# Kernel optimization log

Measured on AMD Instinct MI355X. Metric: run time of the kernel, lower is better.

Reference implementation:

```python
import jax, jax.numpy as jnp
import numpy as np
from jax import lax

B, T, I, H = 256, 256, 512, 512


def setup_inputs() -> dict:
    key = jax.random.key(0)
    ks = jax.random.split(key, 7)
    s = 1.0 / np.sqrt(H)
    return {
        "x": jax.random.normal(ks[0], (B, T, I), dtype=jnp.float32),
        "W_ih": jax.random.normal(ks[1], (4 * H, I), dtype=jnp.float32) * s,
        "W_hh": jax.random.normal(ks[2], (4 * H, H), dtype=jnp.float32) * s,
        "b_ih": jax.random.normal(ks[3], (4 * H,), dtype=jnp.float32) * s,
        "b_hh": jax.random.normal(ks[4], (4 * H,), dtype=jnp.float32) * s,
        "fc_w": jax.random.normal(ks[5], (1, H), dtype=jnp.float32) * s,
        "fc_b": jax.random.normal(ks[6], (1,), dtype=jnp.float32) * s,
    }


def reference(x, W_ih, W_hh, b_ih, b_hh, fc_w, fc_b):
    # x: [B, T, I]. Single-layer LSTM (PyTorch gate order i,f,g,o), zero init state.
    Bh = x.shape[0]
    Hd = W_hh.shape[1]
    # Precompute input contribution for all timesteps: [B, T, 4H]
    xg = jnp.einsum('bti,gi->btg', x, W_ih) + b_ih + b_hh

    def step(carry, xt):
        h, c = carry
        g = xt + h @ W_hh.T  # [B, 4H]
        i = jax.nn.sigmoid(g[:, :Hd])
        f = jax.nn.sigmoid(g[:, Hd:2 * Hd])
        gg = jnp.tanh(g[:, 2 * Hd:3 * Hd])
        o = jax.nn.sigmoid(g[:, 3 * Hd:])
        c_new = f * c + i * gg
        h_new = o * jnp.tanh(c_new)
        return (h_new, c_new), None

    h0 = jnp.zeros((Bh, Hd), dtype=x.dtype)
    c0 = jnp.zeros((Bh, Hd), dtype=x.dtype)
    (h_last, _), _ = lax.scan(step, (h0, c0), jnp.swapaxes(xg, 0, 1))
    # Final linear head on last timestep: [B, 1]
    return h_last @ fc_w.T + fc_b
```

## Files before the change

kernel.cpp:

```cpp
#include <hip/hip_runtime.h>

#define BDIM 256
#define TDIM 256
#define IDIM 512
#define HDIM 512
#define G4   2048

typedef __attribute__((ext_vector_type(4))) float f32x4;
typedef __attribute__((ext_vector_type(8))) short short8;
typedef __attribute__((ext_vector_type(8))) unsigned short u16x8;
typedef __attribute__((ext_vector_type(4))) unsigned short u16x4;
typedef unsigned long long ull;

__device__ __forceinline__ unsigned short f2bf(float f) {
  union { float f; unsigned u; } v; v.f = f;
  unsigned r = v.u + 0x7FFFu + ((v.u >> 16) & 1u);
  return (unsigned short)(r >> 16);
}
__device__ __forceinline__ float bf2f(unsigned short h) {
  union { unsigned u; float f; } v; v.u = ((unsigned)h) << 16; return v.f;
}
__device__ __forceinline__ float sigmoidf_fast(float x) {
  return 1.0f / (1.0f + __expf(-x));
}
__device__ __forceinline__ float tanhf_fast(float x) {
  float e = __expf(2.0f * x);
  return 1.0f - 2.0f / (e + 1.0f);
}
__device__ __forceinline__ void gl_lds16(const unsigned short* g, unsigned short* l) {
  __builtin_amdgcn_global_load_lds(
      (const __attribute__((address_space(1))) unsigned int*)g,
      (__attribute__((address_space(3))) unsigned int*)l, 16, 0, 0);
}

__device__ __forceinline__ size_t xg_off(int m, int n) {
  int b = m >> 8, t = m & 255;
  int q = n >> 9, jcol = n & 511;
  return (((size_t)t * 8 + (b >> 5)) * 8 + (jcol >> 6)) * 8192
         + (size_t)q * 2048 + (b & 31) * 64 + (jcol & 63);
}

__global__ void __launch_bounds__(256) convert_bf16(
    const float* __restrict__ x, const float* __restrict__ w,
    unsigned short* __restrict__ xb, unsigned short* __restrict__ wb)
{
  const size_t NX8 = (size_t)BDIM * TDIM * IDIM / 8;
  const size_t NW8 = (size_t)G4 * IDIM / 8;
  size_t idx = (size_t)blockIdx.x * 256 + threadIdx.x;
  const float4* sp; u16x8* dp; size_t i;
  if (idx < NX8)      { sp = (const float4*)x; dp = (u16x8*)xb; i = idx; }
  else if (idx < NX8 + NW8) { sp = (const float4*)w; dp = (u16x8*)wb; i = idx - NX8; }
  else return;
  float4 a = sp[i * 2], b = sp[i * 2 + 1];
  u16x8 o = { f2bf(a.x), f2bf(a.y), f2bf(a.z), f2bf(a.w),
              f2bf(b.x), f2bf(b.y), f2bf(b.z), f2bf(b.w) };
  dp[i] = o;
}

__global__ void __launch_bounds__(256, 2) xg_gemm_bf16(
    const unsigned short* __restrict__ Xb, const unsigned short* __restrict__ Wb,
    const float* __restrict__ b_ih, const float* __restrict__ b_hh,
    unsigned short* __restrict__ xg)
{
  __shared__ unsigned short sA[128 * 32];
  __shared__ unsigned short sB[128 * 32];

  const int tid  = threadIdx.x;
  const int lane = tid & 63;
  const int wave = tid >> 6;
  const int l15  = lane & 15;
  const int quad = lane >> 4;
  const int nt = blockIdx.x & 15;
  const int mt = blockIdx.x >> 4;
  const int wm = (wave >> 1) * 64;
  const int wn = (wave & 1) * 64;

  f32x4 acc[4][4];
  #pragma unroll
  for (int i = 0; i < 4; ++i)
    #pragma unroll
    for (int j = 0; j < 4; ++j)
      acc[i][j] = (f32x4){0.f, 0.f, 0.f, 0.f};

  for (int kt = 0; kt < 16; ++kt) {
    #pragma unroll
    for (int i = 0; i < 2; ++i) {
      int c   = wave * 128 + i * 64 + lane;
      int row = c >> 2, cg = c & 3;
      const unsigned short* ga = Xb + (size_t)(mt * 128 + row) * 512 + kt * 32 + cg * 8;
      gl_lds16(ga, sA + (size_t)(wave * 128 + i * 64) * 8);
      const unsigned short* gb = Wb + (size_t)(nt * 128 + row) * 512 + kt * 32 + cg * 8;
      gl_lds16(gb, sB + (size_t)(wave * 128 + i * 64) * 8);
    }
    __syncthreads();

    short8 af[4], bfr[4];
    #pragma unroll
    for (int i = 0; i < 4; ++i) {
      af[i]  = *(const short8*)&sA[(wm + i * 16 + l15) * 32 + quad * 8];
      bfr[i] = *(const short8*)&sB[(wn + i * 16 + l15) * 32 + quad * 8];
    }
    #pragma unroll
    for (int am = 0; am < 4; ++am)
      #pragma unroll
      for (int an = 0; an < 4; ++an)
        acc[am][an] = __builtin_amdgcn_mfma_f32_16x16x32_bf16(
            af[am], bfr[an], acc[am][an], 0, 0, 0);
    __syncthreads();
  }

  float biasv[4];
  #pragma unroll
  for (int an = 0; an < 4; ++an) {
    int n = nt * 128 + wn + an * 16 + l15;
    biasv[an] = b_ih[n] + b_hh[n];
  }
  #pragma unroll
  for (int am = 0; am < 4; ++am)
    #pragma unroll
    for (int reg = 0; reg < 4; ++reg) {
      int m = mt * 128 + wm + am * 16 + quad * 4 + reg;
      #pragma unroll
      for (int an = 0; an < 4; ++an) {
        int n = nt * 128 + wn + an * 16 + l15;
        xg[xg_off(m, n)] = f2bf(acc[am][an][reg] + biasv[an]);
      }
    }
}

__global__ void __launch_bounds__(256, 2) xg_gemm_f32(
    const float* __restrict__ X, const float* __restrict__ Wih,
    const float* __restrict__ b_ih, const float* __restrict__ b_hh,
    unsigned short* __restrict__ xg)
{
  __shared__ unsigned short sA[128][40];
  __shared__ unsigned short sB[128][40];

  const int tid  = threadIdx.x;
  const int lane = tid & 63;
  const int wave = tid >> 6;
  const int l15  = lane & 15;
  const int quad = lane >> 4;
  const int nt = blockIdx.x;
  const int mt = blockIdx.y;
  const int wm = (wave >> 1) * 64;
  const int wn = (wave & 1) * 64;
  const int r    = tid >> 1;
  const int half = (tid & 1) * 16;

  const float* arow = X   + (size_t)(mt * 128 + r) * 512 + half;
  const float* brow = Wih + (size_t)(nt * 128 + r) * 512 + half;

  f32x4 acc[4][4];
  #pragma unroll
  for (int i = 0; i < 4; ++i)
    #pragma unroll
    for (int j = 0; j < 4; ++j)
      acc[i][j] = (f32x4){0.f, 0.f, 0.f, 0.f};

  for (int kt = 0; kt < 16; ++kt) {
    const float* ap = arow + kt * 32;
    const float* bp = brow + kt * 32;
    #pragma unroll
    for (int i = 0; i < 4; ++i) {
      float4 a = ((const float4*)ap)[i];
      u16x4 av = { f2bf(a.x), f2bf(a.y), f2bf(a.z), f2bf(a.w) };
      *(u16x4*)&sA[r][half + i * 4] = av;
      float4 b = ((const float4*)bp)[i];
      u16x4 bv = { f2bf(b.x), f2bf(b.y), f2bf(b.z), f2bf(b.w) };
      *(u16x4*)&sB[r][half + i * 4] = bv;
    }
    __syncthreads();
    short8 af[4], bfr[4];
    #pragma unroll
    for (int i = 0; i < 4; ++i) {
      af[i]  = *(const short8*)&sA[wm + i * 16 + l15][quad * 8];
      bfr[i] = *(const short8*)&sB[wn + i * 16 + l15][quad * 8];
    }
    #pragma unroll
    for (int am = 0; am < 4; ++am)
      #pragma unroll
      for (int an = 0; an < 4; ++an)
        acc[am][an] = __builtin_amdgcn_mfma_f32_16x16x32_bf16(
            af[am], bfr[an], acc[am][an], 0, 0, 0);
    __syncthreads();
  }

  float biasv[4];
  #pragma unroll
  for (int an = 0; an < 4; ++an) {
    int n = nt * 128 + wn + an * 16 + l15;
    biasv[an] = b_ih[n] + b_hh[n];
  }
  #pragma unroll
  for (int am = 0; am < 4; ++am)
    #pragma unroll
    for (int reg = 0; reg < 4; ++reg) {
      int m = mt * 128 + wm + am * 16 + quad * 4 + reg;
      #pragma unroll
      for (int an = 0; an < 4; ++an) {
        int n = nt * 128 + wn + an * 16 + l15;
        xg[xg_off(m, n)] = f2bf(acc[am][an][reg] + biasv[an]);
      }
    }
}

__global__ void __launch_bounds__(512, 2) lstm_scan(
    const float* __restrict__ Whh, const unsigned short* __restrict__ xg,
    unsigned short* __restrict__ hbuf0, unsigned short* __restrict__ hbuf1,
    unsigned int* __restrict__ flags)
{
  __shared__ unsigned short sH[32][520];
  __shared__ float sG[32][260];

  const int tid  = threadIdx.x;
  const int lane = tid & 63;
  const int wave = tid >> 6;
  const int l15  = lane & 15;
  const int quad = lane >> 4;
  const int q    = wave >> 1;
  const int np   = (wave & 1) * 2;
  const int bb = blockIdx.x >> 3;
  const int jw = blockIdx.x & 7;
  const int bbase = bb * 32;
  const int jbase = jw * 64;

  short8 bfrag[2][16];
  #pragma unroll
  for (int n2 = 0; n2 < 2; ++n2) {
    const float* wrow = Whh + (size_t)(q * 512 + jbase + (np + n2) * 16 + l15) * 512;
    #pragma unroll
    for (int ks = 0; ks < 16; ++ks) {
      const float* p = wrow + ks * 32 + quad * 8;
      float4 f0 = ((const float4*)p)[0];
      float4 f1 = ((const float4*)p)[1];
      short8 v;
      v[0] = (short)f2bf(f0.x); v[1] = (short)f2bf(f0.y);
      v[2] = (short)f2bf(f0.z); v[3] = (short)f2bf(f0.w);
      v[4] = (short)f2bf(f1.x); v[5] = (short)f2bf(f1.y);
      v[6] = (short)f2bf(f1.z); v[7] = (short)f2bf(f1.w);
      bfrag[n2][ks] = v;
    }
  }

  const int r  = tid >> 4;
  const int j0 = (tid & 15) * 4;
  float c[4] = {0.f, 0.f, 0.f, 0.f};
  unsigned int* flagbase = flags + bb * 32;

  for (int t = 0; t < TDIM; ++t) {
    const unsigned short* hsrc = (t & 1) ? hbuf1 : hbuf0;
    unsigned short* hdst = (t & 1) ? hbuf0 : hbuf1;

    const unsigned short* xgb = xg + (((size_t)t * 8 + bb) * 8 + jw) * 8192;
    ull xv64[4];
    #pragma unroll
    for (int qq = 0; qq < 4; ++qq)
      xv64[qq] = *(const ull*)(xgb + qq * 2048 + r * 64 + j0);

    if (t > 0 && wave == 0) {
      const unsigned int* fp = flagbase + (lane & 7);
      int guard = 0;
      for (;;) {
        unsigned v = __hip_atomic_load(fp, __ATOMIC_RELAXED, __HIP_MEMORY_SCOPE_AGENT);
        bool ok = (lane >= 8) || (v >= (unsigned)t);
        if ((__ballot(ok) & 0xFFull) == 0xFFull) break;
        if (++guard > (1 << 21)) break;
        __builtin_amdgcn_s_sleep(1);
      }
    }
    __syncthreads();

    const ull* src = (const ull*)hsrc + (size_t)bbase * 128;
    ull hv[8];
    #pragma unroll
    for (int i = 0; i < 8; ++i)
      hv[i] = __hip_atomic_load(src + i * 512 + tid, __ATOMIC_RELAXED,
                                __HIP_MEMORY_SCOPE_AGENT);
    #pragma unroll
    for (int i = 0; i < 8; ++i) {
      int idx = i * 512 + tid;
      *(ull*)&sH[idx >> 7][(idx & 127) * 4] = hv[i];
    }
    __syncthreads();

    f32x4 acc[2][2];
    acc[0][0] = acc[0][1] = acc[1][0] = acc[1][1] = (f32x4){0.f,0.f,0.f,0.f};
    #pragma unroll
    for (int ks = 0; ks < 16; ++ks) {
      int koff = ks * 32 + quad * 8;
      short8 a0 = *(const short8*)&sH[l15][koff];
      short8 a1 = *(const short8*)&sH[16 + l15][koff];
      acc[0][0] = __builtin_amdgcn_mfma_f32_16x16x32_bf16(a0, bfrag[0][ks], acc[0][0], 0, 0, 0);
      acc[1][0] = __builtin_amdgcn_mfma_f32_16x16x32_bf16(a1, bfrag[0][ks], acc[1][0], 0, 0, 0);
      acc[0][1] = __builtin_amdgcn_mfma_f32_16x16x32_bf16(a0, bfrag[1][ks], acc[0][1], 0, 0, 0);
      acc[1][1] = __builtin_amdgcn_mfma_f32_16x16x32_bf16(a1, bfrag[1][ks], acc[1][1], 0, 0, 0);
    }
    #pragma unroll
    for (int m = 0; m < 2; ++m)
      #pragma unroll
      for (int n2 = 0; n2 < 2; ++n2) {
        int col = q * 64 + (np + n2) * 16 + l15;
        #pragma unroll
        for (int rr = 0; rr < 4; ++rr)
          sG[m * 16 + quad * 4 + rr][col] = acc[m][n2][rr];
      }
    __syncthreads();

    {
      float4 GI = *(const float4*)&sG[r][j0];
      float4 GF = *(const float4*)&sG[r][64 + j0];
      float4 GG = *(const float4*)&sG[r][128 + j0];
      float4 GO = *(const float4*)&sG[r][192 + j0];
      u16x4 xi  = __builtin_bit_cast(u16x4, xv64[0]);
      u16x4 xf  = __builtin_bit_cast(u16x4, xv64[1]);
      u16x4 xgv = __builtin_bit_cast(u16x4, xv64[2]);
      u16x4 xo  = __builtin_bit_cast(u16x4, xv64[3]);
      float gi[4] = {GI.x, GI.y, GI.z, GI.w};
      float gf[4] = {GF.x, GF.y, GF.z, GF.w};
      float gg[4] = {GG.x, GG.y, GG.z, GG.w};
      float go[4] = {GO.x, GO.y, GO.z, GO.w};
      float h4[4];
      #pragma unroll
      for (int k = 0; k < 4; ++k) {
        float vi = sigmoidf_fast(gi[k] + bf2f(xi[k]));
        float vf = sigmoidf_fast(gf[k] + bf2f(xf[k]));
        float vg = tanhf_fast   (gg[k] + bf2f(xgv[k]));
        float vo = sigmoidf_fast(go[k] + bf2f(xo[k]));
        c[k] = vf * c[k] + vi * vg;
        h4[k] = vo * tanhf_fast(c[k]);
      }
      ull hvout = (ull)f2bf(h4[0])
                | ((ull)f2bf(h4[1]) << 16)
                | ((ull)f2bf(h4[2]) << 32)
                | ((ull)f2bf(h4[3]) << 48);
      __hip_atomic_store((ull*)hdst + (size_t)(bbase + r) * 128 + (jbase + j0) / 4,
                         hvout, __ATOMIC_RELAXED, __HIP_MEMORY_SCOPE_AGENT);
    }

    __syncthreads();
    if (tid == 0)
      __hip_atomic_store(flagbase + jw, (unsigned)(t + 1), __ATOMIC_RELAXED,
                         __HIP_MEMORY_SCOPE_AGENT);
  }
}

__global__ void head_kernel(const unsigned short* __restrict__ h,
                            const float* __restrict__ fc_w,
                            const float* __restrict__ fc_b,
                            float* __restrict__ out)
{
  const int b = blockIdx.x;
  const int lane = threadIdx.x;
  const unsigned short* hr = h + (size_t)b * 512;
  float s = 0.f;
  #pragma unroll
  for (int i = 0; i < 8; ++i) {
    int idx = lane + i * 64;
    s += bf2f(hr[idx]) * fc_w[idx];
  }
  #pragma unroll
  for (int off = 32; off > 0; off >>= 1) s += __shfl_down(s, off);
  if (lane == 0) out[b] = s + fc_b[0];
}

extern "C" void kernel_launch(void* const* d_in, const int* in_sizes, int n_in,
                              void* d_out, int out_size, void* d_ws, size_t ws_size,
                              hipStream_t stream) {
  const float* x    = (const float*)d_in[0];
  const float* W_ih = (const float*)d_in[1];
  const float* W_hh = (const float*)d_in[2];
  const float* b_ih = (const float*)d_in[3];
  const float* b_hh = (const float*)d_in[4];
  const float* fc_w = (const float*)d_in[5];
  const float* fc_b = (const float*)d_in[6];
  float* out = (float*)d_out;

  const size_t XG = (size_t)BDIM * TDIM * G4 * 2;
  const size_t HB = (size_t)BDIM * HDIM * 2;
  char* ws = (char*)d_ws;
  unsigned short* xg    = (unsigned short*)ws;
  unsigned short* hbuf0 = (unsigned short*)(ws + XG);
  unsigned short* hbuf1 = (unsigned short*)(ws + XG + HB);
  unsigned int*   flags = (unsigned int*)(ws + XG + 2 * HB);
  const size_t XB_OFF = XG + 2 * HB + 4096;
  const size_t WB_OFF = XB_OFF + (size_t)BDIM * TDIM * IDIM * 2;
  const size_t NEED   = WB_OFF + (size_t)G4 * IDIM * 2;

  hipMemsetAsync(ws + XG, 0, HB, stream);
  hipMemsetAsync(ws + XG + 2 * HB, 0, 4096, stream);

  if (ws_size >= NEED) {
    unsigned short* xb = (unsigned short*)(ws + XB_OFF);
    unsigned short* wb = (unsigned short*)(ws + WB_OFF);
    convert_bf16<<<16896, 256, 0, stream>>>(x, W_ih, xb, wb);
    xg_gemm_bf16<<<8192, 256, 0, stream>>>(xb, wb, b_ih, b_hh, xg);
  } else {
    xg_gemm_f32<<<dim3(16, 512), 256, 0, stream>>>(x, W_ih, b_ih, b_hh, xg);
  }
  lstm_scan<<<64, 512, 0, stream>>>(W_hh, xg, hbuf0, hbuf1, flags);
  head_kernel<<<BDIM, 64, 0, stream>>>(hbuf0, fc_w, fc_b, out);
}
```

Before: 1.521 ms.

## Replace flag-based step sync with per-word sentinel polling in a 4-slot h ring

The per-block step flags and their polling loop are removed. The hidden state now lives in a ring of four buffers, and each consumer spins directly on the h words it needs until they no longer hold a NaN sentinel. Each thread re-poisons its own word in the slot that will be read two steps later, and the host memsets are replaced by a small init kernel. This removes a __syncthreads barrier and the serial flag-publish handoff from every timestep. The cost is more global atomic traffic and a reliance on no real h value ever matching the sentinel bit pattern.

```diff
diff --git a/kernel.cpp b/kernel.cpp
--- a/kernel.cpp
+++ b/kernel.cpp
@@ -5,6 +5,9 @@
 #define IDIM 512
 #define HDIM 512
 #define G4   2048
+
+#define HBW64 32768ull
+#define SENT  0x7FC07FC07FC07FC0ull
 
 typedef __attribute__((ext_vector_type(4))) float f32x4;
 typedef __attribute__((ext_vector_type(8))) short short8;
@@ -57,6 +60,14 @@
   dp[i] = o;
 }
 
+__global__ void __launch_bounds__(256) init_bufs(unsigned short* __restrict__ hb)
+{
+  size_t i = (size_t)blockIdx.x * 256 + threadIdx.x;
+  ull* b = (ull*)hb;
+  if (i < HBW64)            b[i] = SENT;
+  else if (i < 2 * HBW64)   b[3 * HBW64 + (i - HBW64)] = 0ull;
+}
+
 __global__ void __launch_bounds__(256, 2) xg_gemm_bf16(
     const unsigned short* __restrict__ Xb, const unsigned short* __restrict__ Wb,
     const float* __restrict__ b_ih, const float* __restrict__ b_hh,
@@ -207,8 +218,7 @@
 
 __global__ void __launch_bounds__(512, 2) lstm_scan(
     const float* __restrict__ Whh, const unsigned short* __restrict__ xg,
-    unsigned short* __restrict__ hbuf0, unsigned short* __restrict__ hbuf1,
-    unsigned int* __restrict__ flags)
+    unsigned short* __restrict__ hb)
 {
   __shared__ unsigned short sH[32][520];
   __shared__ float sG[32][260];
@@ -246,11 +256,19 @@
   const int r  = tid >> 4;
   const int j0 = (tid & 15) * 4;
   float c[4] = {0.f, 0.f, 0.f, 0.f};
-  unsigned int* flagbase = flags + bb * 32;
+
+  ull* hb64 = (ull*)hb;
+  const size_t myw = (size_t)(bbase + r) * 128 + (size_t)((jbase + j0) >> 2);
 
   for (int t = 0; t < TDIM; ++t) {
-    const unsigned short* hsrc = (t & 1) ? hbuf1 : hbuf0;
-    unsigned short* hdst = (t & 1) ? hbuf0 : hbuf1;
+    const ull* srcb = hb64 + (size_t)((t + 3) & 3) * HBW64;
+    ull*       dstb = hb64 + (size_t)(t & 3) * HBW64;
+
+    if (t < TDIM - 2) {
+      ull* wipb = hb64 + (size_t)((t + 1) & 3) * HBW64;
+      __hip_atomic_store(wipb + myw, SENT, __ATOMIC_RELAXED,
+                         __HIP_MEMORY_SCOPE_AGENT);
+    }
 
     const unsigned short* xgb = xg + (((size_t)t * 8 + bb) * 8 + jw) * 8192;
     ull xv64[4];
@@ -258,25 +276,24 @@
     for (int qq = 0; qq < 4; ++qq)
       xv64[qq] = *(const ull*)(xgb + qq * 2048 + r * 64 + j0);
 
-    if (t > 0 && wave == 0) {
-      const unsigned int* fp = flagbase + (lane & 7);
-      int guard = 0;
-      for (;;) {
-        unsigned v = __hip_atomic_load(fp, __ATOMIC_RELAXED, __HIP_MEMORY_SCOPE_AGENT);
-        bool ok = (lane >= 8) || (v >= (unsigned)t);
-        if ((__ballot(ok) & 0xFFull) == 0xFFull) break;
-        if (++guard > (1 << 21)) break;
-        __builtin_amdgcn_s_sleep(1);
-      }
-    }
-    __syncthreads();
-
-    const ull* src = (const ull*)hsrc + (size_t)bbase * 128;
+    const ull* src = srcb + (size_t)bbase * 128;
     ull hv[8];
     #pragma unroll
     for (int i = 0; i < 8; ++i)
       hv[i] = __hip_atomic_load(src + i * 512 + tid, __ATOMIC_RELAXED,
                                 __HIP_MEMORY_SCOPE_AGENT);
+    for (int guard = 0; guard < (1 << 18); ++guard) {
+      int bad = 0;
+      #pragma unroll
+      for (int i = 0; i < 8; ++i) bad |= (int)(hv[i] == SENT) << i;
+      if (!bad) break;
+      __builtin_amdgcn_s_sleep(1);
+      #pragma unroll
+      for (int i = 0; i < 8; ++i)
+        if (bad & (1 << i))
+          hv[i] = __hip_atomic_load(src + i * 512 + tid, __ATOMIC_RELAXED,
+                                    __HIP_MEMORY_SCOPE_AGENT);
+    }
     #pragma unroll
     for (int i = 0; i < 8; ++i) {
       int idx = i * 512 + tid;
@@ -334,14 +351,10 @@
                 | ((ull)f2bf(h4[1]) << 16)
                 | ((ull)f2bf(h4[2]) << 32)
                 | ((ull)f2bf(h4[3]) << 48);
-      __hip_atomic_store((ull*)hdst + (size_t)(bbase + r) * 128 + (jbase + j0) / 4,
-                         hvout, __ATOMIC_RELAXED, __HIP_MEMORY_SCOPE_AGENT);
-    }
-
-    __syncthreads();
-    if (tid == 0)
-      __hip_atomic_store(flagbase + jw, (unsigned)(t + 1), __ATOMIC_RELAXED,
+      asm volatile("s_waitcnt vmcnt(0)" ::: "memory");
+      __hip_atomic_store(dstb + myw, hvout, __ATOMIC_RELAXED,
                          __HIP_MEMORY_SCOPE_AGENT);
+    }
   }
 }
 
@@ -376,19 +389,13 @@
   const float* fc_b = (const float*)d_in[6];
   float* out = (float*)d_out;
 
-  const size_t XG = (size_t)BDIM * TDIM * G4 * 2;
-  const size_t HB = (size_t)BDIM * HDIM * 2;
+  const size_t XG  = (size_t)BDIM * TDIM * G4 * 2;
   char* ws = (char*)d_ws;
-  unsigned short* xg    = (unsigned short*)ws;
-  unsigned short* hbuf0 = (unsigned short*)(ws + XG);
-  unsigned short* hbuf1 = (unsigned short*)(ws + XG + HB);
-  unsigned int*   flags = (unsigned int*)(ws + XG + 2 * HB);
-  const size_t XB_OFF = XG + 2 * HB + 4096;
-  const size_t WB_OFF = XB_OFF + (size_t)BDIM * TDIM * IDIM * 2;
+  unsigned short* xg = (unsigned short*)ws;
+  unsigned short* hb = (unsigned short*)(ws + XG);
+  const size_t XB_OFF = XG;
+  const size_t WB_OFF = XG + (size_t)BDIM * TDIM * IDIM * 2;
   const size_t NEED   = WB_OFF + (size_t)G4 * IDIM * 2;
-
-  hipMemsetAsync(ws + XG, 0, HB, stream);
-  hipMemsetAsync(ws + XG + 2 * HB, 0, 4096, stream);
 
   if (ws_size >= NEED) {
     unsigned short* xb = (unsigned short*)(ws + XB_OFF);
@@ -398,6 +405,7 @@
   } else {
     xg_gemm_f32<<<dim3(16, 512), 256, 0, stream>>>(x, W_ih, b_ih, b_hh, xg);
   }
-  lstm_scan<<<64, 512, 0, stream>>>(W_hh, xg, hbuf0, hbuf1, flags);
-  head_kernel<<<BDIM, 64, 0, stream>>>(hbuf0, fc_w, fc_b, out);
-}
+  init_bufs<<<256, 256, 0, stream>>>(hb);
+  lstm_scan<<<64, 512, 0, stream>>>(W_hh, xg, hb);
+  head_kernel<<<BDIM, 64, 0, stream>>>(hb + 3 * (size_t)HBW64 * 4, fc_w, fc_b, out);
+}
```

Measured after the change: 1.489 ms. 1.02x faster.
